# Kernel optimization log

Hardware: AMD Instinct MI355X
Metric: run time of the kernel (lower is better)

Reference implementation:

```python
import jax, jax.numpy as jnp
import numpy as np

N = 100000      # nodes
E = 1600000     # edges (before self-loops)
DIN = 256
D = 128         # dmid == dout
L = 4           # n_layers
ALPHA = 0.5
THETA = 1.0
EPS = 1e-5      # pyg LayerNorm default eps


def setup_inputs() -> dict:
    key = jax.random.key(0)
    ks = jax.random.split(key, 6)
    x = jax.random.normal(ks[0], (N, DIN), jnp.float32)
    edge_index = jax.random.randint(ks[1], (2, E), 0, N)
    lin1_w = jax.random.normal(ks[2], (D, DIN), jnp.float32) * (1.0 / np.sqrt(DIN))
    lin1_b = jnp.zeros((D,), jnp.float32)
    w1 = jax.random.normal(ks[3], (L, D, D), jnp.float32) * (1.0 / np.sqrt(D))
    w2 = jax.random.normal(ks[4], (L, D, D), jnp.float32) * (1.0 / np.sqrt(D))
    norm_w = jnp.ones((D,), jnp.float32)
    norm_b = jnp.zeros((D,), jnp.float32)
    return {"x": x, "edge_index": edge_index, "lin1_w": lin1_w, "lin1_b": lin1_b,
            "w1": w1, "w2": w2, "norm_w": norm_w, "norm_b": norm_b}


def reference(x, edge_index, lin1_w, lin1_b, w1, w2, norm_w, norm_b):
    # --- gcn_norm: add self-loops, symmetric degree normalization ---
    sl = jnp.arange(N)
    row = jnp.concatenate([edge_index[0], sl])  # sources
    col = jnp.concatenate([edge_index[1], sl])  # targets (aggregation index)
    deg = jax.ops.segment_sum(jnp.ones(row.shape[0], jnp.float32), col, num_segments=N)
    dis = jax.lax.rsqrt(deg)  # deg >= 1 thanks to self-loops
    enorm = dis[row] * dis[col]  # [E+N]

    # --- f_0 = relu(lin1(x)); prev_h = 0 so x_0 arg == f_0 ---
    f0 = jax.nn.relu(x @ lin1_w.T + lin1_b)  # [N, D]
    x0 = ALPHA * f0
    f = f0

    for i in range(L):
        beta = float(np.log(THETA / (i + 1) + 1.0))
        # sparse neighbor aggregation: h = A_hat @ f
        h = jax.ops.segment_sum(f[row] * enorm[:, None], col, num_segments=N)
        h = h * (1.0 - ALPHA)
        # shared_weights=False: two separate identity/weight mixes
        out = ((1.0 - beta) * h + beta * (h @ w1[i])
               + (1.0 - beta) * x0 + beta * (x0 @ w2[i]))
        # pyg LayerNorm mode='graph', batch=None: normalize over all nodes+channels
        m = out.mean()
        s = jnp.sqrt(jnp.mean((out - m) ** 2))
        out = (out - m) / (s + EPS) * norm_w + norm_b
        f = jax.nn.relu(out)

    # dmid == dout -> lin2 is Identity
    return jax.nn.relu(f)
```

## Files before the change

### kernel.cpp

```cpp
#include <hip/hip_runtime.h>
#include <math.h>

constexpr int N    = 100000;
constexpr int E    = 1600000;
constexpr int DIN  = 256;
constexpr int D    = 128;
constexpr int L    = 4;
constexpr float EPS = 1e-5f;
constexpr int NPP  = 12500;

typedef __attribute__((ext_vector_type(8))) short bf16x8;
typedef __attribute__((ext_vector_type(4))) float f32x4;

__device__ inline ushort f2b(float f) {
    uint u = __float_as_uint(f);
    uint r = u + 0x7fffu + ((u >> 16) & 1u);
    return (ushort)(r >> 16);
}
__device__ inline float b2f(ushort b) { return __uint_as_float(((uint)b) << 16); }


__global__ void k_count(const int* __restrict__ col, int* __restrict__ cnt) {
    int i = blockIdx.x * 256 + threadIdx.x;
    if (i * 2 + 1 < E) {
        int2 cc = ((const int2*)col)[i];
        atomicAdd(&cnt[cc.x], 1);
        atomicAdd(&cnt[cc.y], 1);
    } else if (i * 2 < E) {
        atomicAdd(&cnt[col[i * 2]], 1);
    }
}

__global__ void k_dis(const int* __restrict__ cnt, float* __restrict__ dis) {
    int n = blockIdx.x * 256 + threadIdx.x;
    if (n < N) dis[n] = rsqrtf((float)cnt[n] + 1.0f);
}

__global__ void k_blocksum(const int* __restrict__ cnt, int* __restrict__ bsum) {
    __shared__ int s[256];
    int base = blockIdx.x * 1024;
    int t = threadIdx.x;
    int a = 0;
    for (int j = 0; j < 4; j++) {
        int idx = base + t * 4 + j;
        if (idx < N) a += cnt[idx];
    }
    s[t] = a; __syncthreads();
    for (int off = 128; off > 0; off >>= 1) {
        if (t < off) s[t] += s[t + off];
        __syncthreads();
    }
    if (t == 0) bsum[blockIdx.x] = s[0];
}

__global__ void k_scan(int* __restrict__ bsum, int nb) {
    __shared__ int s[128];
    int t = threadIdx.x;
    int v = (t < nb) ? bsum[t] : 0;
    s[t] = v; __syncthreads();
    for (int off = 1; off < 128; off <<= 1) {
        int x = (t >= off) ? s[t - off] : 0;
        __syncthreads();
        s[t] += x;
        __syncthreads();
    }
    if (t < nb) bsum[t] = s[t] - v;
}

__global__ void k_offsets(const int* __restrict__ cnt, const int* __restrict__ bsum,
                          int* __restrict__ offs) {
    __shared__ int ls[256];
    int b = blockIdx.x, t = threadIdx.x;
    int base = b * 1024;
    int v[4]; int s = 0;
    for (int j = 0; j < 4; j++) {
        int idx = base + t * 4 + j;
        v[j] = (idx < N) ? cnt[idx] : 0;
        s += v[j];
    }
    ls[t] = s; __syncthreads();
    for (int off = 1; off < 256; off <<= 1) {
        int x = (t >= off) ? ls[t - off] : 0;
        __syncthreads();
        ls[t] += x;
        __syncthreads();
    }
    int excl = ((t == 0) ? 0 : ls[t - 1]) + bsum[b];
    for (int j = 0; j < 4; j++) {
        int idx = base + t * 4 + j;
        if (idx < N) offs[idx] = excl;
        excl += v[j];
        if (idx == N - 1) offs[N] = excl;
    }
}

__global__ void k_scatter(const int* __restrict__ row, const int* __restrict__ col,
                          const float* __restrict__ dis, int* __restrict__ cur,
                          int2* __restrict__ csr) {
    int part = blockIdx.x & 7;
    int base = ((blockIdx.x >> 3) * 256 + threadIdx.x) * 4;
    if (base >= E) return;
    int4 c4 = *(const int4*)(col + base);
    int4 r4 = *(const int4*)(row + base);
    int cs[4] = {c4.x, c4.y, c4.z, c4.w};
    int rs[4] = {r4.x, r4.y, r4.z, r4.w};
    #pragma unroll
    for (int j = 0; j < 4; j++) {
        if (cs[j] / NPP == part) {
            int pos = atomicAdd(&cur[cs[j]], 1);
            csr[pos] = make_int2(rs[j], __float_as_int(dis[rs[j]] * dis[cs[j]]));
        }
    }
}


__global__ void k_prep_w(const float* __restrict__ lin1_w, const float* __restrict__ w1,
                         const float* __restrict__ w2, float4 betas,
                         ushort* __restrict__ wb0, ushort* __restrict__ wbc) {
    int i = blockIdx.x * 256 + threadIdx.x;
    if (i < D * DIN) wb0[i] = f2b(lin1_w[i]);
    if (i < L * D * 256) {
        int l = i >> 15, r = i & 32767, d = r >> 8, k = r & 255;
        float beta = (l == 0) ? betas.x : (l == 1) ? betas.y : (l == 2) ? betas.z : betas.w;
        float v;
        if (k < 128) v = beta * w1[l * 16384 + k * 128 + d] + ((k == d) ? (1.f - beta) : 0.f);
        else { int kk = k - 128; v = beta * w2[l * 16384 + kk * 128 + d] + ((kk == d) ? (1.f - beta) : 0.f); }
        wbc[l * 32768 + d * 256 + k] = f2b(v);
    }
}


__global__ __launch_bounds__(512, 2) void k_f0_mfma(const float* __restrict__ x,
        const ushort* __restrict__ wb, const float* __restrict__ bias,
        ushort* __restrict__ f_bf, ushort* __restrict__ x0_bf) {
    __shared__ uint4 Bl[4096];
    int t = threadIdx.x;
    #pragma unroll
    for (int it = 0; it < 8; it++) {
        int d = it * 512 + t, c = d >> 5, ck = d & 31;
        Bl[c * 32 + (ck ^ (c & 7))] = ((const uint4*)wb)[d];
    }
    __syncthreads();

    int wv = t >> 6, lane = t & 63;
    int l16 = lane & 15, g16 = lane >> 4;
    int row0 = (blockIdx.x * 8 + wv) * 16;
    if (row0 >= N) return;

    const uint4* xb = (const uint4*)(x + (size_t)(row0 + l16) * 256);
    uint4 xr[16];
    #pragma unroll
    for (int ks = 0; ks < 8; ks++) {
        xr[2 * ks]     = xb[ks * 8 + g16 * 2];
        xr[2 * ks + 1] = xb[ks * 8 + g16 * 2 + 1];
    }

    f32x4 acc[8];
    #pragma unroll
    for (int n = 0; n < 8; n++) acc[n] = f32x4{0.f, 0.f, 0.f, 0.f};

    #pragma unroll
    for (int ks = 0; ks < 8; ks++) {
        float4 lo = *(const float4*)&xr[2 * ks];
        float4 hi = *(const float4*)&xr[2 * ks + 1];
        uint4 p;
        p.x = (uint)f2b(lo.x) | ((uint)f2b(lo.y) << 16);
        p.y = (uint)f2b(lo.z) | ((uint)f2b(lo.w) << 16);
        p.z = (uint)f2b(hi.x) | ((uint)f2b(hi.y) << 16);
        p.w = (uint)f2b(hi.z) | ((uint)f2b(hi.w) << 16);
        bf16x8 a = *(bf16x8*)&p;
        int xo = (ks * 4 + g16) ^ (l16 & 7);
        const char* bp = (const char*)Bl + l16 * 512 + xo * 16;
        #pragma unroll
        for (int n = 0; n < 8; n++) {
            bf16x8 b = *(const bf16x8*)(bp + n * 8192);
            acc[n] = __builtin_amdgcn_mfma_f32_16x16x32_bf16(a, b, acc[n], 0, 0, 0);
        }
    }

    float bc[8];
    #pragma unroll
    for (int n = 0; n < 8; n++) bc[n] = bias[n * 16 + l16];
    #pragma unroll
    for (int j = 0; j < 4; j++) {
        int gr = row0 + g16 * 4 + j;
        #pragma unroll
        for (int n = 0; n < 8; n++) {
            float r = fmaxf(acc[n][j] + bc[n], 0.f);
            size_t o = (size_t)gr * 128 + n * 16 + l16;
            f_bf[o] = f2b(r);
            x0_bf[o] = f2b(0.5f * r);
        }
    }
}

__global__ __launch_bounds__(512, 2) void k_combine_mfma(const ushort* __restrict__ g_bf,
        const ushort* __restrict__ x0_bf, const ushort* __restrict__ wb,
        ushort* __restrict__ h_bf, float* __restrict__ sr) {
    __shared__ uint4 Bl[4096];
    __shared__ float red1[512];
    __shared__ float red2[512];
    int t = threadIdx.x;
    #pragma unroll
    for (int it = 0; it < 8; it++) {
        int d = it * 512 + t, c = d >> 5, ck = d & 31;
        Bl[c * 32 + (ck ^ (c & 7))] = ((const uint4*)wb)[d];
    }
    __syncthreads();

    int wv = t >> 6, lane = t & 63;
    int l16 = lane & 15, g16 = lane >> 4;
    int row0 = (blockIdx.x * 8 + wv) * 16;
    bool active = row0 < N;

    f32x4 acc[8];
    #pragma unroll
    for (int n = 0; n < 8; n++) acc[n] = f32x4{0.f, 0.f, 0.f, 0.f};

    if (active) {
        const uint4* ga = (const uint4*)(g_bf  + (size_t)(row0 + l16) * 128);
        const uint4* xa = (const uint4*)(x0_bf + (size_t)(row0 + l16) * 128);
        uint4 ar[8];
        #pragma unroll
        for (int ks = 0; ks < 4; ks++) ar[ks]     = ga[ks * 4 + g16];
        #pragma unroll
        for (int ks = 0; ks < 4; ks++) ar[ks + 4] = xa[ks * 4 + g16];

        #pragma unroll
        for (int ks = 0; ks < 8; ks++) {
            bf16x8 a = *(bf16x8*)&ar[ks];
            int xo = (ks * 4 + g16) ^ (l16 & 7);
            const char* bp = (const char*)Bl + l16 * 512 + xo * 16;
            #pragma unroll
            for (int n = 0; n < 8; n++) {
                bf16x8 b = *(const bf16x8*)(bp + n * 8192);
                acc[n] = __builtin_amdgcn_mfma_f32_16x16x32_bf16(a, b, acc[n], 0, 0, 0);
            }
        }
    }

    float sum = 0.f, sq = 0.f;
    if (active) {
        #pragma unroll
        for (int n = 0; n < 8; n++)
            #pragma unroll
            for (int j = 0; j < 4; j++) { float v = acc[n][j]; sum += v; sq += v * v; }
        #pragma unroll
        for (int j = 0; j < 4; j++) {
            int gr = row0 + g16 * 4 + j;
            #pragma unroll
            for (int n = 0; n < 8; n++)
                h_bf[(size_t)gr * 128 + n * 16 + l16] = f2b(acc[n][j]);
        }
    }

    red1[t] = sum; red2[t] = sq; __syncthreads();
    for (int off = 256; off > 0; off >>= 1) {
        if (t < off) { red1[t] += red1[t + off]; red2[t] += red2[t + off]; }
        __syncthreads();
    }
    if (t == 0) { atomicAdd(&sr[0], red1[0]); atomicAdd(&sr[1], red2[0]); }
}


template <int AFFINE>
__global__ __launch_bounds__(256) void k_agg(const ushort* __restrict__ src,
        const int* __restrict__ offs, const int2* __restrict__ csr,
        const float* __restrict__ dis, const float* __restrict__ sr,
        const float* __restrict__ nw, const float* __restrict__ nb,
        ushort* __restrict__ g_bf) {
    int node = blockIdx.x * 4 + (threadIdx.x >> 6);
    if (node >= N) return;
    int lane = threadIdx.x & 63;
    int q = lane >> 4, cl = lane & 15;
    const uint4* fu = (const uint4*)src;

    float sc[8], sh[8];
    if constexpr (AFFINE) {
        const float inv_n = 1.0f / ((float)N * (float)D);
        float m = sr[0] * inv_n;
        float var = fmaxf(sr[1] * inv_n - m * m, 0.f);
        float inv = 1.0f / (sqrtf(var) + EPS);
        #pragma unroll
        for (int j = 0; j < 8; j++) {
            float w = nw[cl * 8 + j];
            sc[j] = inv * w;
            sh[j] = nb[cl * 8 + j] - m * inv * w;
        }
    }

    float a[8];
    #pragma unroll
    for (int j = 0; j < 8; j++) a[j] = 0.f;

    auto acc8 = [&](float val, uint4 rv) {
        uint vv[4] = {rv.x, rv.y, rv.z, rv.w};
        #pragma unroll
        for (int j2 = 0; j2 < 4; j2++) {
            float lo = b2f((ushort)(vv[j2] & 0xffffu));
            float hi = b2f((ushort)(vv[j2] >> 16));
            if constexpr (AFFINE) {
                lo = fmaxf(fmaf(lo, sc[2 * j2], sh[2 * j2]), 0.f);
                hi = fmaxf(fmaf(hi, sc[2 * j2 + 1], sh[2 * j2 + 1]), 0.f);
            }
            a[2 * j2]     += val * lo;
            a[2 * j2 + 1] += val * hi;
        }
    };

    float dv = dis[node];
    acc8((q == 0) ? dv * dv : 0.f, fu[(size_t)node * 16 + cl]);

    int end = offs[node + 1];
    int i = offs[node] + q * 2;
    if (i < end) {
        int iA = i;
        int2 rA0 = csr[iA];
        int2 rA1 = csr[min(iA + 1, end - 1)];
        uint4 wA0 = fu[(size_t)rA0.x * 16 + cl];
        uint4 wA1 = fu[(size_t)rA1.x * 16 + cl];
        for (int iB = iA + 8; iB < end; iB += 8) {
            int2 rB0 = csr[iB];
            int2 rB1 = csr[min(iB + 1, end - 1)];
            uint4 wB0 = fu[(size_t)rB0.x * 16 + cl];
            uint4 wB1 = fu[(size_t)rB1.x * 16 + cl];
            acc8(__int_as_float(rA0.y), wA0);
            acc8(__int_as_float(rA1.y), wA1);
            iA = iB; rA0 = rB0; rA1 = rB1; wA0 = wB0; wA1 = wB1;
        }
        acc8(__int_as_float(rA0.y), wA0);
        if (iA + 1 < end) acc8(__int_as_float(rA1.y), wA1);
    }

    #pragma unroll
    for (int j = 0; j < 8; j++) {
        a[j] += __shfl_xor(a[j], 16, 64);
        a[j] += __shfl_xor(a[j], 32, 64);
    }
    if (q == 0) {
        uint4 o;
        o.x = (uint)f2b(0.5f * a[0]) | ((uint)f2b(0.5f * a[1]) << 16);
        o.y = (uint)f2b(0.5f * a[2]) | ((uint)f2b(0.5f * a[3]) << 16);
        o.z = (uint)f2b(0.5f * a[4]) | ((uint)f2b(0.5f * a[5]) << 16);
        o.w = (uint)f2b(0.5f * a[6]) | ((uint)f2b(0.5f * a[7]) << 16);
        ((uint4*)g_bf)[(size_t)node * 16 + cl] = o;
    }
}


__global__ void k_ln_final(const ushort* __restrict__ ob, const float* __restrict__ sr,
                           const float* __restrict__ nw, const float* __restrict__ nb,
                           float* __restrict__ fout) {
    int i = blockIdx.x * 256 + threadIdx.x;
    if (i >= N * 16) return;
    const float inv_n = 1.0f / ((float)N * (float)D);
    float m = sr[0] * inv_n;
    float var = fmaxf(sr[1] * inv_n - m * m, 0.f);
    float inv = 1.0f / (sqrtf(var) + EPS);
    uint4 v = ((const uint4*)ob)[i];
    int c = (i & 15) * 8;
    uint vv[4] = {v.x, v.y, v.z, v.w};
    float r[8];
    #pragma unroll
    for (int qd = 0; qd < 4; qd++) {
        float lo = b2f((ushort)(vv[qd] & 0xffff));
        float hi = b2f((ushort)(vv[qd] >> 16));
        r[2 * qd]     = fmaxf((lo - m) * inv * nw[c + 2 * qd]     + nb[c + 2 * qd], 0.f);
        r[2 * qd + 1] = fmaxf((hi - m) * inv * nw[c + 2 * qd + 1] + nb[c + 2 * qd + 1], 0.f);
    }
    float4 o0 = {r[0], r[1], r[2], r[3]};
    float4 o1 = {r[4], r[5], r[6], r[7]};
    ((float4*)fout)[2 * i] = o0;
    ((float4*)fout)[2 * i + 1] = o1;
}


extern "C" void kernel_launch(void* const* d_in, const int* in_sizes, int n_in,
                              void* d_out, int out_size, void* d_ws, size_t ws_size,
                              hipStream_t stream) {
    const float* x      = (const float*)d_in[0];
    const int*   ei     = (const int*)d_in[1];
    const float* lin1_w = (const float*)d_in[2];
    const float* lin1_b = (const float*)d_in[3];
    const float* w1     = (const float*)d_in[4];
    const float* w2     = (const float*)d_in[5];
    const float* nw     = (const float*)d_in[6];
    const float* nb     = (const float*)d_in[7];
    const int* row = ei;
    const int* col = ei + E;
    float* fout = (float*)d_out;

    char* ws = (char*)d_ws;
    size_t off0 = 0;
    auto alloc = [&](size_t bytes) -> char* {
        char* p = ws + off0;
        off0 = (off0 + bytes + 255) & ~(size_t)255;
        return p;
    };
    ushort* f_bf    = (ushort*)alloc((size_t)N * D * 2);
    ushort* x0_bf   = (ushort*)alloc((size_t)N * D * 2);
    ushort* g_bf    = (ushort*)alloc((size_t)N * D * 2);
    ushort* h_bf    = (ushort*)alloc((size_t)N * D * 2);
    float*  dis     = (float*) alloc((size_t)N * 4);
    int*    cnt     = (int*)   alloc((size_t)N * 4);
    int*    offs    = (int*)   alloc((size_t)(N + 1) * 4);
    int*    cur     = (int*)   alloc((size_t)N * 4);
    int*    bsum    = (int*)   alloc((size_t)128 * 4);
    int2*   csr     = (int2*)  alloc((size_t)E * 8);
    float*  stats   = (float*) alloc(64);
    ushort* wb0     = (ushort*)alloc((size_t)D * DIN * 2);
    ushort* wbc     = (ushort*)alloc((size_t)L * D * 256 * 2);

    hipMemsetAsync(cnt, 0, (size_t)N * 4, stream);
    hipMemsetAsync(stats, 0, 64, stream);

    k_count<<<(E / 2 + 255) / 256, 256, 0, stream>>>(col, cnt);
    k_dis<<<(N + 255) / 256, 256, 0, stream>>>(cnt, dis);
    int nbk = (N + 1023) / 1024;
    k_blocksum<<<nbk, 256, 0, stream>>>(cnt, bsum);
    k_scan<<<1, 128, 0, stream>>>(bsum, nbk);
    k_offsets<<<nbk, 256, 0, stream>>>(cnt, bsum, offs);
    hipMemcpyAsync(cur, offs, (size_t)N * 4, hipMemcpyDeviceToDevice, stream);
    int echunks = (E / 4 + 255) / 256;
    k_scatter<<<echunks * 8, 256, 0, stream>>>(row, col, dis, cur, csr);

    float4 betas;
    betas.x = logf(1.0f / 1.0f + 1.0f);
    betas.y = logf(1.0f / 2.0f + 1.0f);
    betas.z = logf(1.0f / 3.0f + 1.0f);
    betas.w = logf(1.0f / 4.0f + 1.0f);
    k_prep_w<<<(L * D * 256 + 255) / 256, 256, 0, stream>>>(lin1_w, w1, w2, betas, wb0, wbc);

    int GB = (N / 16 + 7) / 8;
    k_f0_mfma<<<GB, 512, 0, stream>>>(x, wb0, lin1_b, f_bf, x0_bf);

    int AGB = (N + 3) / 4;
    for (int i = 0; i < L; i++) {
        if (i == 0)
            k_agg<0><<<AGB, 256, 0, stream>>>(f_bf, offs, csr, dis, nullptr, nw, nb, g_bf);
        else
            k_agg<1><<<AGB, 256, 0, stream>>>(h_bf, offs, csr, dis, stats + 2 * (i - 1), nw, nb, g_bf);
        k_combine_mfma<<<GB, 512, 0, stream>>>(g_bf, x0_bf, wbc + (size_t)i * D * 256,
                                               h_bf, stats + 2 * i);
    }
    k_ln_final<<<(N * 16 + 255) / 256, 256, 0, stream>>>(h_bf, stats + 6, nw, nb, fout);
}
```

Measured before the change: 573.7 us.

## Fuse sparse aggregation into MFMA combine kernel, move LayerNorm to separate pass

Each layer's sparse gather runs inside the MFMA combine kernel. Every lane aggregates neighbour rows directly into the A-operand fragment layout, so the g_bf intermediate buffer and its write and read are gone. Because the gather no longer applies the affine LayerNorm and ReLU on the fly, a separate elementwise k_ln_relu pass now rewrites f_bf in bf16 for each layer, adding a full read and write per layer. Per-edge gather parallelism also changes from 4 edge streams per node to one serial chain per lane group, and the CSR scatter now uses nontemporal 64-bit stores.

```diff
diff --git a/kernel.cpp b/kernel.cpp
--- a/kernel.cpp
+++ b/kernel.cpp
@@ -11,6 +11,7 @@
 
 typedef __attribute__((ext_vector_type(8))) short bf16x8;
 typedef __attribute__((ext_vector_type(4))) float f32x4;
+typedef __attribute__((ext_vector_type(2))) float f32x2;
 
 __device__ inline ushort f2b(float f) {
     uint u = __float_as_uint(f);
@@ -96,7 +97,7 @@
 
 __global__ void k_scatter(const int* __restrict__ row, const int* __restrict__ col,
                           const float* __restrict__ dis, int* __restrict__ cur,
-                          int2* __restrict__ csr) {
+                          unsigned long long* __restrict__ csr) {
     int part = blockIdx.x & 7;
     int base = ((blockIdx.x >> 3) * 256 + threadIdx.x) * 4;
     if (base >= E) return;
@@ -108,7 +109,9 @@
     for (int j = 0; j < 4; j++) {
         if (cs[j] / NPP == part) {
             int pos = atomicAdd(&cur[cs[j]], 1);
-            csr[pos] = make_int2(rs[j], __float_as_int(dis[rs[j]] * dis[cs[j]]));
+            unsigned long long rec = (unsigned int)rs[j]
+                | ((unsigned long long)__float_as_uint(dis[rs[j]] * dis[cs[j]]) << 32);
+            __builtin_nontemporal_store(rec, csr + pos);
         }
     }
 }
@@ -194,9 +197,12 @@
     }
 }
 
-__global__ __launch_bounds__(512, 2) void k_combine_mfma(const ushort* __restrict__ g_bf,
-        const ushort* __restrict__ x0_bf, const ushort* __restrict__ wb,
-        ushort* __restrict__ h_bf, float* __restrict__ sr) {
+
+__global__ __launch_bounds__(512, 2) void k_layer(const ushort* __restrict__ f_bf,
+        const ushort* __restrict__ x0_bf, const int* __restrict__ offs,
+        const int2* __restrict__ csr, const float* __restrict__ dis,
+        const ushort* __restrict__ wb, ushort* __restrict__ h_bf,
+        float* __restrict__ sr) {
     __shared__ uint4 Bl[4096];
     __shared__ float red1[512];
     __shared__ float red2[512];
@@ -213,22 +219,93 @@
     int row0 = (blockIdx.x * 8 + wv) * 16;
     bool active = row0 < N;
 
-    f32x4 acc[8];
-    #pragma unroll
-    for (int n = 0; n < 8; n++) acc[n] = f32x4{0.f, 0.f, 0.f, 0.f};
+    float sum = 0.f, sq = 0.f;
 
     if (active) {
-        const uint4* ga = (const uint4*)(g_bf  + (size_t)(row0 + l16) * 128);
         const uint4* xa = (const uint4*)(x0_bf + (size_t)(row0 + l16) * 128);
-        uint4 ar[8];
-        #pragma unroll
-        for (int ks = 0; ks < 4; ks++) ar[ks]     = ga[ks * 4 + g16];
-        #pragma unroll
-        for (int ks = 0; ks < 4; ks++) ar[ks + 4] = xa[ks * 4 + g16];
-
+        uint4 xr[4];
+        #pragma unroll
+        for (int ks = 0; ks < 4; ks++) xr[ks] = xa[ks * 4 + g16];
+
+        const uint4* fu = (const uint4*)f_bf;
+        int node = row0 + l16;
+
+        f32x2 ga[4][4];
+        #pragma unroll
+        for (int k = 0; k < 4; k++)
+            #pragma unroll
+            for (int p = 0; p < 4; p++) ga[k][p] = f32x2{0.f, 0.f};
+
+        auto ld4 = [&](int r, uint4 (&w)[4]) {
+            const uint4* p = fu + (size_t)r * 16 + g16;
+            w[0] = p[0]; w[1] = p[4]; w[2] = p[8]; w[3] = p[12];
+        };
+        auto acc4 = [&](float val, const uint4 (&w)[4]) {
+            f32x2 v2 = {val, val};
+            #pragma unroll
+            for (int k = 0; k < 4; k++) {
+                uint uu[4] = {w[k].x, w[k].y, w[k].z, w[k].w};
+                #pragma unroll
+                for (int p = 0; p < 4; p++) {
+                    f32x2 c;
+                    c.x = __uint_as_float(uu[p] << 16);
+                    c.y = __uint_as_float(uu[p] & 0xffff0000u);
+                    ga[k][p] = __builtin_elementwise_fma(v2, c, ga[k][p]);
+                }
+            }
+        };
+
+        {
+            float dv = dis[node];
+            uint4 w[4];
+            ld4(node, w);
+            acc4(dv * dv, w);
+        }
+
+        int e = offs[node], end = offs[node + 1];
+        int2 r0, r1, r2, r3;
+        uint4 w0[4], w1[4];
+        if (e < end)     { r0 = csr[e];     ld4(r0.x, w0); }
+        if (e + 1 < end) { r1 = csr[e + 1]; ld4(r1.x, w1); }
+        if (e + 2 < end) r2 = csr[e + 2];
+        if (e + 3 < end) r3 = csr[e + 3];
+        int i = e;
+        while (i + 5 < end) {
+            int2 ra = csr[i + 4];
+            int2 rb = csr[i + 5];
+            acc4(__int_as_float(r0.y), w0);
+            ld4(r2.x, w0);
+            acc4(__int_as_float(r1.y), w1);
+            ld4(r3.x, w1);
+            r0 = r2; r1 = r3; r2 = ra; r3 = rb;
+            i += 2;
+        }
+        if (i < end)     acc4(__int_as_float(r0.y), w0);
+        if (i + 1 < end) acc4(__int_as_float(r1.y), w1);
+        for (int j = i + 2; j < end; j++) {
+            int2 rr = csr[j];
+            uint4 ww[4];
+            ld4(rr.x, ww);
+            acc4(__int_as_float(rr.y), ww);
+        }
+
+        bf16x8 ag[4];
+        #pragma unroll
+        for (int ks = 0; ks < 4; ks++) {
+            uint4 pw;
+            pw.x = (uint)f2b(0.5f * ga[ks][0].x) | ((uint)f2b(0.5f * ga[ks][0].y) << 16);
+            pw.y = (uint)f2b(0.5f * ga[ks][1].x) | ((uint)f2b(0.5f * ga[ks][1].y) << 16);
+            pw.z = (uint)f2b(0.5f * ga[ks][2].x) | ((uint)f2b(0.5f * ga[ks][2].y) << 16);
+            pw.w = (uint)f2b(0.5f * ga[ks][3].x) | ((uint)f2b(0.5f * ga[ks][3].y) << 16);
+            ag[ks] = *(bf16x8*)&pw;
+        }
+
+        f32x4 acc[8];
+        #pragma unroll
+        for (int n = 0; n < 8; n++) acc[n] = f32x4{0.f, 0.f, 0.f, 0.f};
         #pragma unroll
         for (int ks = 0; ks < 8; ks++) {
-            bf16x8 a = *(bf16x8*)&ar[ks];
+            bf16x8 a = (ks < 4) ? ag[ks] : *(bf16x8*)&xr[ks - 4];
             int xo = (ks * 4 + g16) ^ (l16 & 7);
             const char* bp = (const char*)Bl + l16 * 512 + xo * 16;
             #pragma unroll
@@ -237,10 +314,7 @@
                 acc[n] = __builtin_amdgcn_mfma_f32_16x16x32_bf16(a, b, acc[n], 0, 0, 0);
             }
         }
-    }
-
-    float sum = 0.f, sq = 0.f;
-    if (active) {
+
         #pragma unroll
         for (int n = 0; n < 8; n++)
             #pragma unroll
@@ -263,94 +337,10 @@
 }
 
 
-template <int AFFINE>
-__global__ __launch_bounds__(256) void k_agg(const ushort* __restrict__ src,
-        const int* __restrict__ offs, const int2* __restrict__ csr,
-        const float* __restrict__ dis, const float* __restrict__ sr,
-        const float* __restrict__ nw, const float* __restrict__ nb,
-        ushort* __restrict__ g_bf) {
-    int node = blockIdx.x * 4 + (threadIdx.x >> 6);
-    if (node >= N) return;
-    int lane = threadIdx.x & 63;
-    int q = lane >> 4, cl = lane & 15;
-    const uint4* fu = (const uint4*)src;
-
-    float sc[8], sh[8];
-    if constexpr (AFFINE) {
-        const float inv_n = 1.0f / ((float)N * (float)D);
-        float m = sr[0] * inv_n;
-        float var = fmaxf(sr[1] * inv_n - m * m, 0.f);
-        float inv = 1.0f / (sqrtf(var) + EPS);
-        #pragma unroll
-        for (int j = 0; j < 8; j++) {
-            float w = nw[cl * 8 + j];
-            sc[j] = inv * w;
-            sh[j] = nb[cl * 8 + j] - m * inv * w;
-        }
-    }
-
-    float a[8];
-    #pragma unroll
-    for (int j = 0; j < 8; j++) a[j] = 0.f;
-
-    auto acc8 = [&](float val, uint4 rv) {
-        uint vv[4] = {rv.x, rv.y, rv.z, rv.w};
-        #pragma unroll
-        for (int j2 = 0; j2 < 4; j2++) {
-            float lo = b2f((ushort)(vv[j2] & 0xffffu));
-            float hi = b2f((ushort)(vv[j2] >> 16));
-            if constexpr (AFFINE) {
-                lo = fmaxf(fmaf(lo, sc[2 * j2], sh[2 * j2]), 0.f);
-                hi = fmaxf(fmaf(hi, sc[2 * j2 + 1], sh[2 * j2 + 1]), 0.f);
-            }
-            a[2 * j2]     += val * lo;
-            a[2 * j2 + 1] += val * hi;
-        }
-    };
-
-    float dv = dis[node];
-    acc8((q == 0) ? dv * dv : 0.f, fu[(size_t)node * 16 + cl]);
-
-    int end = offs[node + 1];
-    int i = offs[node] + q * 2;
-    if (i < end) {
-        int iA = i;
-        int2 rA0 = csr[iA];
-        int2 rA1 = csr[min(iA + 1, end - 1)];
-        uint4 wA0 = fu[(size_t)rA0.x * 16 + cl];
-        uint4 wA1 = fu[(size_t)rA1.x * 16 + cl];
-        for (int iB = iA + 8; iB < end; iB += 8) {
-            int2 rB0 = csr[iB];
-            int2 rB1 = csr[min(iB + 1, end - 1)];
-            uint4 wB0 = fu[(size_t)rB0.x * 16 + cl];
-            uint4 wB1 = fu[(size_t)rB1.x * 16 + cl];
-            acc8(__int_as_float(rA0.y), wA0);
-            acc8(__int_as_float(rA1.y), wA1);
-            iA = iB; rA0 = rB0; rA1 = rB1; wA0 = wB0; wA1 = wB1;
-        }
-        acc8(__int_as_float(rA0.y), wA0);
-        if (iA + 1 < end) acc8(__int_as_float(rA1.y), wA1);
-    }
-
-    #pragma unroll
-    for (int j = 0; j < 8; j++) {
-        a[j] += __shfl_xor(a[j], 16, 64);
-        a[j] += __shfl_xor(a[j], 32, 64);
-    }
-    if (q == 0) {
-        uint4 o;
-        o.x = (uint)f2b(0.5f * a[0]) | ((uint)f2b(0.5f * a[1]) << 16);
-        o.y = (uint)f2b(0.5f * a[2]) | ((uint)f2b(0.5f * a[3]) << 16);
-        o.z = (uint)f2b(0.5f * a[4]) | ((uint)f2b(0.5f * a[5]) << 16);
-        o.w = (uint)f2b(0.5f * a[6]) | ((uint)f2b(0.5f * a[7]) << 16);
-        ((uint4*)g_bf)[(size_t)node * 16 + cl] = o;
-    }
-}
-
-
-__global__ void k_ln_final(const ushort* __restrict__ ob, const float* __restrict__ sr,
-                           const float* __restrict__ nw, const float* __restrict__ nb,
-                           float* __restrict__ fout) {
+template <int LAST>
+__global__ void k_ln_relu(const ushort* __restrict__ ob, const float* __restrict__ sr,
+                          const float* __restrict__ nw, const float* __restrict__ nb,
+                          ushort* __restrict__ f_bf, float* __restrict__ fout) {
     int i = blockIdx.x * 256 + threadIdx.x;
     if (i >= N * 16) return;
     const float inv_n = 1.0f / ((float)N * (float)D);
@@ -368,10 +358,19 @@
         r[2 * qd]     = fmaxf((lo - m) * inv * nw[c + 2 * qd]     + nb[c + 2 * qd], 0.f);
         r[2 * qd + 1] = fmaxf((hi - m) * inv * nw[c + 2 * qd + 1] + nb[c + 2 * qd + 1], 0.f);
     }
-    float4 o0 = {r[0], r[1], r[2], r[3]};
-    float4 o1 = {r[4], r[5], r[6], r[7]};
-    ((float4*)fout)[2 * i] = o0;
-    ((float4*)fout)[2 * i + 1] = o1;
+    if (LAST) {
+        float4 o0 = {r[0], r[1], r[2], r[3]};
+        float4 o1 = {r[4], r[5], r[6], r[7]};
+        ((float4*)fout)[2 * i] = o0;
+        ((float4*)fout)[2 * i + 1] = o1;
+    } else {
+        uint4 o;
+        o.x = (uint)f2b(r[0]) | ((uint)f2b(r[1]) << 16);
+        o.y = (uint)f2b(r[2]) | ((uint)f2b(r[3]) << 16);
+        o.z = (uint)f2b(r[4]) | ((uint)f2b(r[5]) << 16);
+        o.w = (uint)f2b(r[6]) | ((uint)f2b(r[7]) << 16);
+        ((uint4*)f_bf)[i] = o;
+    }
 }
 
 
@@ -399,7 +398,6 @@
     };
     ushort* f_bf    = (ushort*)alloc((size_t)N * D * 2);
     ushort* x0_bf   = (ushort*)alloc((size_t)N * D * 2);
-    ushort* g_bf    = (ushort*)alloc((size_t)N * D * 2);
     ushort* h_bf    = (ushort*)alloc((size_t)N * D * 2);
     float*  dis     = (float*) alloc((size_t)N * 4);
     int*    cnt     = (int*)   alloc((size_t)N * 4);
@@ -422,7 +420,8 @@
     k_offsets<<<nbk, 256, 0, stream>>>(cnt, bsum, offs);
     hipMemcpyAsync(cur, offs, (size_t)N * 4, hipMemcpyDeviceToDevice, stream);
     int echunks = (E / 4 + 255) / 256;
-    k_scatter<<<echunks * 8, 256, 0, stream>>>(row, col, dis, cur, csr);
+    k_scatter<<<echunks * 8, 256, 0, stream>>>(row, col, dis, cur,
+                                               (unsigned long long*)csr);
 
     float4 betas;
     betas.x = logf(1.0f / 1.0f + 1.0f);
@@ -434,14 +433,13 @@
     int GB = (N / 16 + 7) / 8;
     k_f0_mfma<<<GB, 512, 0, stream>>>(x, wb0, lin1_b, f_bf, x0_bf);
 
-    int AGB = (N + 3) / 4;
+    int LNB = (N * 16 + 255) / 256;
     for (int i = 0; i < L; i++) {
-        if (i == 0)
-            k_agg<0><<<AGB, 256, 0, stream>>>(f_bf, offs, csr, dis, nullptr, nw, nb, g_bf);
+        k_layer<<<GB, 512, 0, stream>>>(f_bf, x0_bf, offs, csr, dis,
+                                        wbc + (size_t)i * D * 256, h_bf, stats + 2 * i);
+        if (i < L - 1)
+            k_ln_relu<0><<<LNB, 256, 0, stream>>>(h_bf, stats + 2 * i, nw, nb, f_bf, nullptr);
         else
-            k_agg<1><<<AGB, 256, 0, stream>>>(h_bf, offs, csr, dis, stats + 2 * (i - 1), nw, nb, g_bf);
-        k_combine_mfma<<<GB, 512, 0, stream>>>(g_bf, x0_bf, wbc + (size_t)i * D * 256,
-                                               h_bf, stats + 2 * i);
-    }
-    k_ln_final<<<(N * 16 + 255) / 256, 256, 0, stream>>>(h_bf, stats + 6, nw, nb, fout);
-}
+            k_ln_relu<1><<<LNB, 256, 0, stream>>>(h_bf, stats + 2 * i, nw, nb, nullptr, fout);
+    }
+}
```

New measurement: 604.7 us. 5.4% more time.

## Unfuse LayerNorm from aggregation into separate pass, use packed FMA accumulation

Applied to the files above, without the earlier changes.

The LayerNorm affine and ReLU, previously applied per gathered neighbour inside the aggregation kernel, now run once per node in a separate elementwise pass that writes bf16 features. The aggregation loop is also rewritten to use packed two-wide FMAs on bf16 values unpacked by shifts, and the CSR scatter uses nontemporal 64-bit stores. This removes redundant per-edge normalization arithmetic (about 17 gathers per node) at the cost of three extra full-array read/write passes.

```diff
diff --git a/kernel.cpp b/kernel.cpp
--- a/kernel.cpp
+++ b/kernel.cpp
@@ -11,6 +11,7 @@
 
 typedef __attribute__((ext_vector_type(8))) short bf16x8;
 typedef __attribute__((ext_vector_type(4))) float f32x4;
+typedef __attribute__((ext_vector_type(2))) float f32x2;
 
 __device__ inline ushort f2b(float f) {
     uint u = __float_as_uint(f);
@@ -96,7 +97,7 @@
 
 __global__ void k_scatter(const int* __restrict__ row, const int* __restrict__ col,
                           const float* __restrict__ dis, int* __restrict__ cur,
-                          int2* __restrict__ csr) {
+                          unsigned long long* __restrict__ csr) {
     int part = blockIdx.x & 7;
     int base = ((blockIdx.x >> 3) * 256 + threadIdx.x) * 4;
     if (base >= E) return;
@@ -108,7 +109,9 @@
     for (int j = 0; j < 4; j++) {
         if (cs[j] / NPP == part) {
             int pos = atomicAdd(&cur[cs[j]], 1);
-            csr[pos] = make_int2(rs[j], __float_as_int(dis[rs[j]] * dis[cs[j]]));
+            unsigned long long rec = (unsigned int)rs[j]
+                | ((unsigned long long)__float_as_uint(dis[rs[j]] * dis[cs[j]]) << 32);
+            __builtin_nontemporal_store(rec, csr + pos);
         }
     }
 }
@@ -194,6 +197,7 @@
     }
 }
 
+
 __global__ __launch_bounds__(512, 2) void k_combine_mfma(const ushort* __restrict__ g_bf,
         const ushort* __restrict__ x0_bf, const ushort* __restrict__ wb,
         ushort* __restrict__ h_bf, float* __restrict__ sr) {
@@ -263,48 +267,28 @@
 }
 
 
-template <int AFFINE>
 __global__ __launch_bounds__(256) void k_agg(const ushort* __restrict__ src,
         const int* __restrict__ offs, const int2* __restrict__ csr,
-        const float* __restrict__ dis, const float* __restrict__ sr,
-        const float* __restrict__ nw, const float* __restrict__ nb,
-        ushort* __restrict__ g_bf) {
+        const float* __restrict__ dis, ushort* __restrict__ g_bf) {
     int node = blockIdx.x * 4 + (threadIdx.x >> 6);
     if (node >= N) return;
     int lane = threadIdx.x & 63;
     int q = lane >> 4, cl = lane & 15;
     const uint4* fu = (const uint4*)src;
 
-    float sc[8], sh[8];
-    if constexpr (AFFINE) {
-        const float inv_n = 1.0f / ((float)N * (float)D);
-        float m = sr[0] * inv_n;
-        float var = fmaxf(sr[1] * inv_n - m * m, 0.f);
-        float inv = 1.0f / (sqrtf(var) + EPS);
-        #pragma unroll
-        for (int j = 0; j < 8; j++) {
-            float w = nw[cl * 8 + j];
-            sc[j] = inv * w;
-            sh[j] = nb[cl * 8 + j] - m * inv * w;
-        }
-    }
-
-    float a[8];
-    #pragma unroll
-    for (int j = 0; j < 8; j++) a[j] = 0.f;
+    f32x2 a2[4];
+    #pragma unroll
+    for (int p = 0; p < 4; p++) a2[p] = f32x2{0.f, 0.f};
 
     auto acc8 = [&](float val, uint4 rv) {
-        uint vv[4] = {rv.x, rv.y, rv.z, rv.w};
-        #pragma unroll
-        for (int j2 = 0; j2 < 4; j2++) {
-            float lo = b2f((ushort)(vv[j2] & 0xffffu));
-            float hi = b2f((ushort)(vv[j2] >> 16));
-            if constexpr (AFFINE) {
-                lo = fmaxf(fmaf(lo, sc[2 * j2], sh[2 * j2]), 0.f);
-                hi = fmaxf(fmaf(hi, sc[2 * j2 + 1], sh[2 * j2 + 1]), 0.f);
-            }
-            a[2 * j2]     += val * lo;
-            a[2 * j2 + 1] += val * hi;
+        uint uu[4] = {rv.x, rv.y, rv.z, rv.w};
+        f32x2 v2 = {val, val};
+        #pragma unroll
+        for (int p = 0; p < 4; p++) {
+            f32x2 c;
+            c.x = __uint_as_float(uu[p] << 16);
+            c.y = __uint_as_float(uu[p] & 0xffff0000u);
+            a2[p] = __builtin_elementwise_fma(v2, c, a2[p]);
         }
     };
 
@@ -333,24 +317,27 @@
     }
 
     #pragma unroll
-    for (int j = 0; j < 8; j++) {
-        a[j] += __shfl_xor(a[j], 16, 64);
-        a[j] += __shfl_xor(a[j], 32, 64);
+    for (int p = 0; p < 4; p++) {
+        a2[p].x += __shfl_xor(a2[p].x, 16, 64);
+        a2[p].x += __shfl_xor(a2[p].x, 32, 64);
+        a2[p].y += __shfl_xor(a2[p].y, 16, 64);
+        a2[p].y += __shfl_xor(a2[p].y, 32, 64);
     }
     if (q == 0) {
         uint4 o;
-        o.x = (uint)f2b(0.5f * a[0]) | ((uint)f2b(0.5f * a[1]) << 16);
-        o.y = (uint)f2b(0.5f * a[2]) | ((uint)f2b(0.5f * a[3]) << 16);
-        o.z = (uint)f2b(0.5f * a[4]) | ((uint)f2b(0.5f * a[5]) << 16);
-        o.w = (uint)f2b(0.5f * a[6]) | ((uint)f2b(0.5f * a[7]) << 16);
+        o.x = (uint)f2b(0.5f * a2[0].x) | ((uint)f2b(0.5f * a2[0].y) << 16);
+        o.y = (uint)f2b(0.5f * a2[1].x) | ((uint)f2b(0.5f * a2[1].y) << 16);
+        o.z = (uint)f2b(0.5f * a2[2].x) | ((uint)f2b(0.5f * a2[2].y) << 16);
+        o.w = (uint)f2b(0.5f * a2[3].x) | ((uint)f2b(0.5f * a2[3].y) << 16);
         ((uint4*)g_bf)[(size_t)node * 16 + cl] = o;
     }
 }
 
 
-__global__ void k_ln_final(const ushort* __restrict__ ob, const float* __restrict__ sr,
-                           const float* __restrict__ nw, const float* __restrict__ nb,
-                           float* __restrict__ fout) {
+template <int LAST>
+__global__ void k_ln_relu(const ushort* __restrict__ ob, const float* __restrict__ sr,
+                          const float* __restrict__ nw, const float* __restrict__ nb,
+                          ushort* __restrict__ f_bf, float* __restrict__ fout) {
     int i = blockIdx.x * 256 + threadIdx.x;
     if (i >= N * 16) return;
     const float inv_n = 1.0f / ((float)N * (float)D);
@@ -368,10 +355,19 @@
         r[2 * qd]     = fmaxf((lo - m) * inv * nw[c + 2 * qd]     + nb[c + 2 * qd], 0.f);
         r[2 * qd + 1] = fmaxf((hi - m) * inv * nw[c + 2 * qd + 1] + nb[c + 2 * qd + 1], 0.f);
     }
-    float4 o0 = {r[0], r[1], r[2], r[3]};
-    float4 o1 = {r[4], r[5], r[6], r[7]};
-    ((float4*)fout)[2 * i] = o0;
-    ((float4*)fout)[2 * i + 1] = o1;
+    if (LAST) {
+        float4 o0 = {r[0], r[1], r[2], r[3]};
+        float4 o1 = {r[4], r[5], r[6], r[7]};
+        ((float4*)fout)[2 * i] = o0;
+        ((float4*)fout)[2 * i + 1] = o1;
+    } else {
+        uint4 o;
+        o.x = (uint)f2b(r[0]) | ((uint)f2b(r[1]) << 16);
+        o.y = (uint)f2b(r[2]) | ((uint)f2b(r[3]) << 16);
+        o.z = (uint)f2b(r[4]) | ((uint)f2b(r[5]) << 16);
+        o.w = (uint)f2b(r[6]) | ((uint)f2b(r[7]) << 16);
+        ((uint4*)f_bf)[i] = o;
+    }
 }
 
 
@@ -422,7 +418,8 @@
     k_offsets<<<nbk, 256, 0, stream>>>(cnt, bsum, offs);
     hipMemcpyAsync(cur, offs, (size_t)N * 4, hipMemcpyDeviceToDevice, stream);
     int echunks = (E / 4 + 255) / 256;
-    k_scatter<<<echunks * 8, 256, 0, stream>>>(row, col, dis, cur, csr);
+    k_scatter<<<echunks * 8, 256, 0, stream>>>(row, col, dis, cur,
+                                               (unsigned long long*)csr);
 
     float4 betas;
     betas.x = logf(1.0f / 1.0f + 1.0f);
@@ -435,13 +432,14 @@
     k_f0_mfma<<<GB, 512, 0, stream>>>(x, wb0, lin1_b, f_bf, x0_bf);
 
     int AGB = (N + 3) / 4;
+    int LNB = (N * 16 + 255) / 256;
     for (int i = 0; i < L; i++) {
-        if (i == 0)
-            k_agg<0><<<AGB, 256, 0, stream>>>(f_bf, offs, csr, dis, nullptr, nw, nb, g_bf);
-        else
-            k_agg<1><<<AGB, 256, 0, stream>>>(h_bf, offs, csr, dis, stats + 2 * (i - 1), nw, nb, g_bf);
+        k_agg<<<AGB, 256, 0, stream>>>(f_bf, offs, csr, dis, g_bf);
         k_combine_mfma<<<GB, 512, 0, stream>>>(g_bf, x0_bf, wbc + (size_t)i * D * 256,
                                                h_bf, stats + 2 * i);
-    }
-    k_ln_final<<<(N * 16 + 255) / 256, 256, 0, stream>>>(h_bf, stats + 6, nw, nb, fout);
-}
+        if (i < L - 1)
+            k_ln_relu<0><<<LNB, 256, 0, stream>>>(h_bf, stats + 2 * i, nw, nb, f_bf, nullptr);
+        else
+            k_ln_relu<1><<<LNB, 256, 0, stream>>>(h_bf, stats + 2 * i, nw, nb, nullptr, fout);
+    }
+}
```

Measured after the change: 599.8 us. 4.5% more time.
